# Performance work log

Hardware: AMD Instinct MI355X
Metric: run time of the kernel (lower is better)

Reference implementation:

```python
import jax, jax.numpy as jnp
import numpy as np

B, S, N, F_IN = 4, 256, 500, 32
D, L = 64, 2
TEMP = 0.5
EPS = 1e-5

def gelu(x):
    return jax.nn.gelu(x, approximate=False)  # torch default GELU (erf)

def layernorm(h, g, b):
    mu = h.mean(-1, keepdims=True)
    var = ((h - mu) ** 2).mean(-1, keepdims=True)
    return (h - mu) * jax.lax.rsqrt(var + EPS) * g + b

def gru_last(x_seq, Wih, Whh, bih, bhh):
    # x_seq: [B, T, I]; torch nn.GRU gate math, h0 = 0; returns final hidden [B, D]
    xp = jnp.einsum('bti,gi->btg', x_seq, Wih) + bih  # precompute input gates [B, T, 3D]
    d = Whh.shape[1]
    def step(h, xpt):
        gh = h @ Whh.T + bhh
        xr, xz, xn = jnp.split(xpt, 3, axis=-1)
        hr, hz, hn = jnp.split(gh, 3, axis=-1)
        r = jax.nn.sigmoid(xr + hr)
        z = jax.nn.sigmoid(xz + hz)
        n = jnp.tanh(xn + r * hn)
        return (1.0 - z) * n + z * h, None
    h0 = jnp.zeros((x_seq.shape[0], d), x_seq.dtype)
    h, _ = jax.lax.scan(step, h0, xp.transpose(1, 0, 2))
    return h

def forward(x, ip_W, ip_b, from_embed, to_embed, gl_W, gl_b, gl_g, gl_be,
            Wih_s, Whh_s, bih_s, bhh_s, Wih_m, Whh_m, bih_m, bhh_m,
            Wih_l, Whh_l, bih_l, bhh_l, dh_W1, dh_b1, dh_W2, dh_b2):
    # input_proj: Linear + GELU (Dropout is identity in eval)
    x = gelu(jnp.einsum('bsnf,df->bsnd', x, ip_W) + ip_b)  # [B,S,N,D]
    # learned adjacency: softmax over destination nodes
    adj = jax.nn.softmax((from_embed @ to_embed.T) / TEMP, axis=-1)  # [N,N]
    for i in range(gl_W.shape[0]):
        agg = jnp.einsum('bsnd,nm->bsmd', x, adj)
        h = gelu(jnp.einsum('bsnd,ed->bsne', x + agg, gl_W[i]) + gl_b[i])
        x = layernorm(h, gl_g[i], gl_be[i])
    b, s, n, d = x.shape
    x_flat = x.reshape(b, s, n * d)
    h_s = gru_last(x_flat[:, -10:, :], Wih_s, Whh_s, bih_s, bhh_s)
    h_m = gru_last(x_flat[:, -20:, :], Wih_m, Whh_m, bih_m, bhh_m)
    h_l = gru_last(x_flat, Wih_l, Whh_l, bih_l, bhh_l)
    h = jnp.concatenate([h_s, h_m, h_l], axis=-1)  # [B, 3D]
    h = gelu(h @ dh_W1.T + dh_b1)
    return h @ dh_W2.T + dh_b2  # direction logits [B, N]

def setup_inputs():
    key = jax.random.key(0)
    it = iter(jax.random.split(key, 40))
    rn = lambda shape, s=0.02: jax.random.normal(next(it), shape, jnp.float32) * s
    I = N * D
    return {
        'x': jax.random.normal(next(it), (B, S, N, F_IN), jnp.float32),
        'ip_W': rn((D, F_IN)), 'ip_b': jnp.zeros((D,), jnp.float32),
        'from_embed': rn((N, 32), 0.1), 'to_embed': rn((N, 32), 0.1),
        'gl_W': rn((L, D, D)), 'gl_b': jnp.zeros((L, D), jnp.float32),
        'gl_g': jnp.ones((L, D), jnp.float32), 'gl_be': jnp.zeros((L, D), jnp.float32),
        'Wih_s': rn((3 * D, I)), 'Whh_s': rn((3 * D, D)),
        'bih_s': jnp.zeros((3 * D,), jnp.float32), 'bhh_s': jnp.zeros((3 * D,), jnp.float32),
        'Wih_m': rn((3 * D, I)), 'Whh_m': rn((3 * D, D)),
        'bih_m': jnp.zeros((3 * D,), jnp.float32), 'bhh_m': jnp.zeros((3 * D,), jnp.float32),
        'Wih_l': rn((3 * D, I)), 'Whh_l': rn((3 * D, D)),
        'bih_l': jnp.zeros((3 * D,), jnp.float32), 'bhh_l': jnp.zeros((3 * D,), jnp.float32),
        'dh_W1': rn((D, 3 * D)), 'dh_b1': jnp.zeros((D,), jnp.float32),
        'dh_W2': rn((N, D)), 'dh_b2': jnp.zeros((N,), jnp.float32),
    }

def reference(x, ip_W, ip_b, from_embed, to_embed, gl_W, gl_b, gl_g, gl_be,
              Wih_s, Whh_s, bih_s, bhh_s, Wih_m, Whh_m, bih_m, bhh_m,
              Wih_l, Whh_l, bih_l, bhh_l, dh_W1, dh_b1, dh_W2, dh_b2):
    return forward(x, ip_W, ip_b, from_embed, to_embed, gl_W, gl_b, gl_g, gl_be,
                   Wih_s, Whh_s, bih_s, bhh_s, Wih_m, Whh_m, bih_m, bhh_m,
                   Wih_l, Whh_l, bih_l, bhh_l, dh_W1, dh_b1, dh_W2, dh_b2)
```

## Files before the change

### kernel.cpp

```cpp
#include <hip/hip_runtime.h>
#include <math.h>

#define NN 500
#define DD 64
#define NPAD 512
#define COLS 65536
#define BS_TOT 1024
#define I_DIM 32000
#define KS_GRU 40
#define KSL 800

typedef __attribute__((ext_vector_type(8))) short bf16x8;
typedef __attribute__((ext_vector_type(4))) float f32x4;

__device__ __forceinline__ float gelu_f(float x) {
    return 0.5f * x * (1.0f + erff(x * 0.70710678118654752440f));
}

__device__ __forceinline__ unsigned short bf16_rn(float x) {
    unsigned int u = __float_as_uint(x);
    unsigned int r = u + 0x7FFFu + ((u >> 16) & 1u);
    return (unsigned short)(r >> 16);
}
__device__ __forceinline__ float bf16_tof(unsigned short h) {
    return __uint_as_float(((unsigned int)h) << 16);
}
__device__ __forceinline__ unsigned int pack_hl(float x) {
    unsigned short h = bf16_rn(x);
    unsigned short l = bf16_rn(x - bf16_tof(h));
    return (unsigned int)h | ((unsigned int)l << 16);
}
__device__ __forceinline__ float unpack_val(unsigned int u) {
    return __uint_as_float(u << 16) + __uint_as_float(u & 0xFFFF0000u);
}
__device__ __forceinline__ void split4(float4 v, short4& h4, short4& l4) {
    h4.x = (short)bf16_rn(v.x); l4.x = (short)bf16_rn(v.x - bf16_tof((unsigned short)h4.x));
    h4.y = (short)bf16_rn(v.y); l4.y = (short)bf16_rn(v.y - bf16_tof((unsigned short)h4.y));
    h4.z = (short)bf16_rn(v.z); l4.z = (short)bf16_rn(v.z - bf16_tof((unsigned short)h4.z));
    h4.w = (short)bf16_rn(v.w); l4.w = (short)bf16_rn(v.w - bf16_tof((unsigned short)h4.w));
}

__device__ __forceinline__ int swz_k(int row, int kbyte) {
    return kbyte ^ (((row >> 3) & 3) << 4);
}

__global__ __launch_bounds__(512)
void adj_kernel(const float* __restrict__ fe, const float* __restrict__ te,
                short* __restrict__ adjTh, short* __restrict__ adjTl)
{
    __shared__ float fr[32];
    __shared__ float red[8];
    __shared__ float red2[8];
    const int n = blockIdx.x;
    const int tid = threadIdx.x;
    if (tid < 32) fr[tid] = fe[n * 32 + tid];
    __syncthreads();
    const int m = tid;
    float s = -1e30f;
    if (m < NN) {
        float acc = 0.f;
        #pragma unroll
        for (int f = 0; f < 32; ++f) acc += fr[f] * te[m * 32 + f];
        s = acc * 2.0f;
    }
    float v = s;
    #pragma unroll
    for (int off = 32; off; off >>= 1) v = fmaxf(v, __shfl_xor(v, off));
    if ((tid & 63) == 0) red[tid >> 6] = v;
    __syncthreads();
    float bmax = red[0];
    #pragma unroll
    for (int i = 1; i < 8; ++i) bmax = fmaxf(bmax, red[i]);
    float e = (m < NN) ? expf(s - bmax) : 0.f;
    float v2 = e;
    #pragma unroll
    for (int off = 32; off; off >>= 1) v2 += __shfl_xor(v2, off);
    if ((tid & 63) == 0) red2[tid >> 6] = v2;
    __syncthreads();
    float bsum = 0.f;
    #pragma unroll
    for (int i = 0; i < 8; ++i) bsum += red2[i];
    if (m < NN) {
        float p = e / bsum;
        unsigned short h = bf16_rn(p);
        adjTh[(size_t)m * NPAD + n] = (short)h;
        adjTl[(size_t)m * NPAD + n] = (short)bf16_rn(p - bf16_tof(h));
    }
}

__global__ __launch_bounds__(256)
void wsplit_kernel(const float* __restrict__ W, short* __restrict__ H,
                   short* __restrict__ L, int n4)
{
    int i = blockIdx.x * 256 + threadIdx.x;
    if (i < n4) {
        float4 v = *(const float4*)&W[i * 4];
        short4 h4, l4;
        split4(v, h4, l4);
        *(short4*)&H[i * 4] = h4;
        *(short4*)&L[i * 4] = l4;
    }
}

__global__ __launch_bounds__(256)
void proj_mfma_kernel(const float* __restrict__ xin,
                      const short* __restrict__ Wh, const short* __restrict__ Wl,
                      const float* __restrict__ ipb, unsigned int* __restrict__ Xhl)
{
    const int tid  = threadIdx.x;
    const int lane = tid & 63;
    const int wave = tid >> 6;
    const int q = lane >> 4, r16 = lane & 15;
    const size_t row0 = (size_t)blockIdx.x * 128 + wave * 32;

    float bB[4];
    #pragma unroll
    for (int ci = 0; ci < 4; ++ci) bB[ci] = ipb[ci * 16 + r16];

    bf16x8 wh[4], wl[4];
    #pragma unroll
    for (int ci = 0; ci < 4; ++ci) {
        int off = (ci * 16 + r16) * 32 + q * 8;
        wh[ci] = *(const bf16x8*)&Wh[off];
        wl[ci] = *(const bf16x8*)&Wl[off];
    }

    f32x4 acc[2][4];
    #pragma unroll
    for (int i = 0; i < 2; ++i)
        #pragma unroll
        for (int j = 0; j < 4; ++j) acc[i][j] = (f32x4){0.f, 0.f, 0.f, 0.f};

    #pragma unroll
    for (int mi = 0; mi < 2; ++mi) {
        const size_t row = row0 + mi * 16 + r16;
        const int n = (int)(row >> 10), bs = (int)(row & 1023);
        const float* src = &xin[((size_t)bs * NN + n) * 32 + q * 8];
        float4 v0 = *(const float4*)src;
        float4 v1 = *(const float4*)(src + 4);
        short4 h0, l0, h1, l1;
        split4(v0, h0, l0);
        split4(v1, h1, l1);
        bf16x8 ah, al;
        ah[0] = h0.x; ah[1] = h0.y; ah[2] = h0.z; ah[3] = h0.w;
        ah[4] = h1.x; ah[5] = h1.y; ah[6] = h1.z; ah[7] = h1.w;
        al[0] = l0.x; al[1] = l0.y; al[2] = l0.z; al[3] = l0.w;
        al[4] = l1.x; al[5] = l1.y; al[6] = l1.z; al[7] = l1.w;
        #pragma unroll
        for (int ci = 0; ci < 4; ++ci) {
            acc[mi][ci] = __builtin_amdgcn_mfma_f32_16x16x32_bf16(ah, wh[ci], acc[mi][ci], 0, 0, 0);
            acc[mi][ci] = __builtin_amdgcn_mfma_f32_16x16x32_bf16(ah, wl[ci], acc[mi][ci], 0, 0, 0);
            acc[mi][ci] = __builtin_amdgcn_mfma_f32_16x16x32_bf16(al, wh[ci], acc[mi][ci], 0, 0, 0);
        }
    }

    #pragma unroll
    for (int mi = 0; mi < 2; ++mi) {
        #pragma unroll
        for (int rg = 0; rg < 4; ++rg) {
            size_t grow = row0 + mi * 16 + q * 4 + rg;
            #pragma unroll
            for (int ci = 0; ci < 4; ++ci) {
                float y = gelu_f(acc[mi][ci][rg] + bB[ci]);
                Xhl[grow * 64 + ci * 16 + r16] = pack_hl(y);
            }
        }
    }
}

__global__ __launch_bounds__(256)
void agg_mfma_kernel(const unsigned int* __restrict__ Xhl,
                     const short* __restrict__ adjTh, const short* __restrict__ adjTl,
                     unsigned int* __restrict__ Yhl)
{
    __shared__ __align__(16) short Ah[2][128 * 40];
    __shared__ __align__(16) short Al[2][128 * 40];
    __shared__ __align__(16) short Bh[2][128 * 40];
    __shared__ __align__(16) short Bl[2][128 * 40];

    const int tid  = threadIdx.x;
    const int lane = tid & 63;
    const int wave = tid >> 6;
    const int wm = (wave >> 1) * 64;
    const int wc = (wave & 1) * 64;
    const int q = lane >> 4, r16 = lane & 15;
    const int c0 = blockIdx.x * 128;
    const int m0 = blockIdx.y * 128;

    const int sa_m = tid >> 1, sa_kh = tid & 1;
    const int sb_c = tid & 127, sb_kh = tid >> 7;
    const size_t cb = (size_t)(c0 + sb_c);

    f32x4 acc[4][4];
    #pragma unroll
    for (int i = 0; i < 4; ++i)
        #pragma unroll
        for (int j = 0; j < 4; ++j) acc[i][j] = (f32x4){0.f, 0.f, 0.f, 0.f};

    {
        const size_t base = (size_t)(m0 + sa_m) * NPAD + sa_kh * 16;
        bf16x8 h0 = *(const bf16x8*)&adjTh[base];
        bf16x8 h1 = *(const bf16x8*)&adjTh[base + 8];
        bf16x8 l0 = *(const bf16x8*)&adjTl[base];
        bf16x8 l1 = *(const bf16x8*)&adjTl[base + 8];
        char* rowH = (char*)Ah[0] + sa_m * 80;
        char* rowL = (char*)Al[0] + sa_m * 80;
        *(bf16x8*)(rowH + swz_k(sa_m, sa_kh * 32))      = h0;
        *(bf16x8*)(rowH + swz_k(sa_m, sa_kh * 32 + 16)) = h1;
        *(bf16x8*)(rowL + swz_k(sa_m, sa_kh * 32))      = l0;
        *(bf16x8*)(rowL + swz_k(sa_m, sa_kh * 32 + 16)) = l1;

        unsigned int u[16];
        #pragma unroll
        for (int j = 0; j < 16; ++j) {
            int kk = sb_kh * 16 + j;
            u[j] = (kk < NN) ? Xhl[(size_t)kk * COLS + cb] : 0u;
        }
        bf16x8 bh0, bh1, bl0, bl1;
        #pragma unroll
        for (int j = 0; j < 8; ++j) {
            bh0[j] = (short)(u[j] & 0xFFFFu);     bl0[j] = (short)(u[j] >> 16);
            bh1[j] = (short)(u[8 + j] & 0xFFFFu); bl1[j] = (short)(u[8 + j] >> 16);
        }
        char* rbH = (char*)Bh[0] + sb_c * 80;
        char* rbL = (char*)Bl[0] + sb_c * 80;
        int kb0 = swz_k(sb_c, sb_kh * 32);
        int kb1 = swz_k(sb_c, sb_kh * 32 + 16);
        *(bf16x8*)(rbH + kb0) = bh0; *(bf16x8*)(rbH + kb1) = bh1;
        *(bf16x8*)(rbL + kb0) = bl0; *(bf16x8*)(rbL + kb1) = bl1;
    }
    __syncthreads();

    for (int kc = 0; kc < 16; ++kc) {
        const int cur = kc & 1;
        bf16x8 nAh0, nAh1, nAl0, nAl1;
        unsigned int nu[16];
        if (kc < 15) {
            const int k0n = (kc + 1) * 32;
            const size_t base = (size_t)(m0 + sa_m) * NPAD + k0n + sa_kh * 16;
            nAh0 = *(const bf16x8*)&adjTh[base];
            nAh1 = *(const bf16x8*)&adjTh[base + 8];
            nAl0 = *(const bf16x8*)&adjTl[base];
            nAl1 = *(const bf16x8*)&adjTl[base + 8];
            #pragma unroll
            for (int j = 0; j < 16; ++j) {
                int kk = k0n + sb_kh * 16 + j;
                nu[j] = (kk < NN) ? Xhl[(size_t)kk * COLS + cb] : 0u;
            }
        }
        bf16x8 ah[4], al[4];
        #pragma unroll
        for (int mi = 0; mi < 4; ++mi) {
            int row = wm + mi * 16 + r16;
            int kb = swz_k(row, q * 16);
            ah[mi] = *(const bf16x8*)((const char*)Ah[cur] + row * 80 + kb);
            al[mi] = *(const bf16x8*)((const char*)Al[cur] + row * 80 + kb);
        }
        #pragma unroll
        for (int ci = 0; ci < 4; ++ci) {
            int row = wc + ci * 16 + r16;
            int kb = swz_k(row, q * 16);
            bf16x8 bh = *(const bf16x8*)((const char*)Bh[cur] + row * 80 + kb);
            bf16x8 bl = *(const bf16x8*)((const char*)Bl[cur] + row * 80 + kb);
            #pragma unroll
            for (int mi = 0; mi < 4; ++mi) {
                acc[mi][ci] = __builtin_amdgcn_mfma_f32_16x16x32_bf16(ah[mi], bh, acc[mi][ci], 0, 0, 0);
                acc[mi][ci] = __builtin_amdgcn_mfma_f32_16x16x32_bf16(ah[mi], bl, acc[mi][ci], 0, 0, 0);
                acc[mi][ci] = __builtin_amdgcn_mfma_f32_16x16x32_bf16(al[mi], bh, acc[mi][ci], 0, 0, 0);
            }
        }
        if (kc < 15) {
            const int nb = cur ^ 1;
            char* rowH = (char*)Ah[nb] + sa_m * 80;
            char* rowL = (char*)Al[nb] + sa_m * 80;
            *(bf16x8*)(rowH + swz_k(sa_m, sa_kh * 32))      = nAh0;
            *(bf16x8*)(rowH + swz_k(sa_m, sa_kh * 32 + 16)) = nAh1;
            *(bf16x8*)(rowL + swz_k(sa_m, sa_kh * 32))      = nAl0;
            *(bf16x8*)(rowL + swz_k(sa_m, sa_kh * 32 + 16)) = nAl1;
            bf16x8 bh0, bh1, bl0, bl1;
            #pragma unroll
            for (int j = 0; j < 8; ++j) {
                bh0[j] = (short)(nu[j] & 0xFFFFu);     bl0[j] = (short)(nu[j] >> 16);
                bh1[j] = (short)(nu[8 + j] & 0xFFFFu); bl1[j] = (short)(nu[8 + j] >> 16);
            }
            char* rbH = (char*)Bh[nb] + sb_c * 80;
            char* rbL = (char*)Bl[nb] + sb_c * 80;
            int kb0 = swz_k(sb_c, sb_kh * 32);
            int kb1 = swz_k(sb_c, sb_kh * 32 + 16);
            *(bf16x8*)(rbH + kb0) = bh0; *(bf16x8*)(rbH + kb1) = bh1;
            *(bf16x8*)(rbL + kb0) = bl0; *(bf16x8*)(rbL + kb1) = bl1;
        }
        __syncthreads();
    }

    #pragma unroll
    for (int mi = 0; mi < 4; ++mi) {
        #pragma unroll
        for (int r = 0; r < 4; ++r) {
            int m = m0 + wm + mi * 16 + q * 4 + r;
            if (m < NN) {
                #pragma unroll
                for (int ci = 0; ci < 4; ++ci) {
                    size_t idx = (size_t)m * COLS + c0 + wc + ci * 16 + r16;
                    float y = acc[mi][ci][r] + unpack_val(Xhl[idx]);
                    Yhl[idx] = pack_hl(y);
                }
            }
        }
    }
}

__global__ __launch_bounds__(256)
void hln_stream_kernel(unsigned int* __restrict__ Xio,
                       const short* __restrict__ Wh, const short* __restrict__ Wl,
                       const float* __restrict__ glb, const float* __restrict__ glg,
                       const float* __restrict__ glbe)
{
    const int tid  = threadIdx.x;
    const int lane = tid & 63;
    const int wave = tid >> 6;
    const int q = lane >> 4, r16 = lane & 15;
    const size_t row0 = (size_t)blockIdx.x * 128 + wave * 32;

    float bB2[4], bG2[4], bE2[4];
    #pragma unroll
    for (int ci = 0; ci < 4; ++ci) {
        int e = ci * 16 + r16;
        bB2[ci] = glb[e]; bG2[ci] = glg[e]; bE2[ci] = glbe[e];
    }

    f32x4 acc[2][4];
    #pragma unroll
    for (int i = 0; i < 2; ++i)
        #pragma unroll
        for (int j = 0; j < 4; ++j) acc[i][j] = (f32x4){0.f, 0.f, 0.f, 0.f};

    #pragma unroll
    for (int kh = 0; kh < 2; ++kh) {
        bf16x8 wh[4], wl[4];
        #pragma unroll
        for (int ci = 0; ci < 4; ++ci) {
            int off = (ci * 16 + r16) * 64 + kh * 32 + q * 8;
            wh[ci] = *(const bf16x8*)&Wh[off];
            wl[ci] = *(const bf16x8*)&Wl[off];
        }
        #pragma unroll
        for (int mi = 0; mi < 2; ++mi) {
            const size_t row = row0 + mi * 16 + r16;
            const unsigned int* src = &Xio[row * 64 + kh * 32 + q * 8];
            uint4 u0 = *(const uint4*)src;
            uint4 u1 = *(const uint4*)(src + 4);
            bf16x8 ah, al;
            ah[0] = (short)(u0.x & 0xFFFFu); al[0] = (short)(u0.x >> 16);
            ah[1] = (short)(u0.y & 0xFFFFu); al[1] = (short)(u0.y >> 16);
            ah[2] = (short)(u0.z & 0xFFFFu); al[2] = (short)(u0.z >> 16);
            ah[3] = (short)(u0.w & 0xFFFFu); al[3] = (short)(u0.w >> 16);
            ah[4] = (short)(u1.x & 0xFFFFu); al[4] = (short)(u1.x >> 16);
            ah[5] = (short)(u1.y & 0xFFFFu); al[5] = (short)(u1.y >> 16);
            ah[6] = (short)(u1.z & 0xFFFFu); al[6] = (short)(u1.z >> 16);
            ah[7] = (short)(u1.w & 0xFFFFu); al[7] = (short)(u1.w >> 16);
            #pragma unroll
            for (int ci = 0; ci < 4; ++ci) {
                acc[mi][ci] = __builtin_amdgcn_mfma_f32_16x16x32_bf16(ah, wh[ci], acc[mi][ci], 0, 0, 0);
                acc[mi][ci] = __builtin_amdgcn_mfma_f32_16x16x32_bf16(ah, wl[ci], acc[mi][ci], 0, 0, 0);
                acc[mi][ci] = __builtin_amdgcn_mfma_f32_16x16x32_bf16(al, wh[ci], acc[mi][ci], 0, 0, 0);
            }
        }
    }

    #pragma unroll
    for (int mi = 0; mi < 2; ++mi) {
        #pragma unroll
        for (int rg = 0; rg < 4; ++rg) {
            float h[4];
            float s1 = 0.f;
            #pragma unroll
            for (int ci = 0; ci < 4; ++ci) {
                h[ci] = gelu_f(acc[mi][ci][rg] + bB2[ci]);
                s1 += h[ci];
            }
            #pragma unroll
            for (int off = 1; off < 16; off <<= 1) s1 += __shfl_xor(s1, off);
            float mu = s1 * (1.f / 64.f);
            float s2 = 0.f;
            #pragma unroll
            for (int ci = 0; ci < 4; ++ci) { float dc = h[ci] - mu; s2 += dc * dc; }
            #pragma unroll
            for (int off = 1; off < 16; off <<= 1) s2 += __shfl_xor(s2, off);
            float rs = 1.f / sqrtf(s2 * (1.f / 64.f) + 1e-5f);
            size_t grow = row0 + mi * 16 + q * 4 + rg;
            #pragma unroll
            for (int ci = 0; ci < 4; ++ci) {
                float y = (h[ci] - mu) * rs * bG2[ci] + bE2[ci];
                Xio[grow * 64 + ci * 16 + r16] = pack_hl(y);
            }
        }
    }
}

__global__ __launch_bounds__(256)
void wconv_kernel(const float* __restrict__ W0, const float* __restrict__ W1,
                  const float* __restrict__ W2,
                  short* __restrict__ h0, short* __restrict__ l0,
                  short* __restrict__ h1, short* __restrict__ l1,
                  short* __restrict__ h2, short* __restrict__ l2)
{
    const int gi = blockIdx.y;
    const float* W = (gi == 0) ? W0 : (gi == 1) ? W1 : W2;
    short* H = (gi == 0) ? h0 : (gi == 1) ? h1 : h2;
    short* L = (gi == 0) ? l0 : (gi == 1) ? l1 : l2;
    const size_t i = ((size_t)blockIdx.x * 256 + threadIdx.x) * 4;
    float4 v = *(const float4*)&W[i];
    short4 h4, l4;
    split4(v, h4, l4);
    *(short4*)&H[i] = h4;
    *(short4*)&L[i] = l4;
}

__global__ __launch_bounds__(256)
void gru_pre_mfma_kernel(const unsigned int* __restrict__ Xhl,
                         const short* __restrict__ Wh0, const short* __restrict__ Wl0,
                         const short* __restrict__ Wh1, const short* __restrict__ Wl1,
                         const short* __restrict__ Wh2, const short* __restrict__ Wl2,
                         float* __restrict__ p0, float* __restrict__ p1,
                         float* __restrict__ p2)
{
    __shared__ __align__(16) short Ah[64 * 40];
    __shared__ __align__(16) short Al[64 * 40];
    __shared__ __align__(16) short Bh[192 * 40];
    __shared__ __align__(16) short Bl[192 * 40];

    const int bid = blockIdx.x;
    int gi, mtid, ks;
    if (bid < 40)       { gi = 0; mtid = 0;             ks = bid; }
    else if (bid < 120) { int r = bid - 40;  gi = 1; ks = r % 40; mtid = r / 40; }
    else                { int r = bid - 120; gi = 2; ks = r % 40; mtid = r / 40; }
    const short* Wh = (gi == 0) ? Wh0 : (gi == 1) ? Wh1 : Wh2;
    const short* Wl = (gi == 0) ? Wl0 : (gi == 1) ? Wl1 : Wl2;
    float* partial  = (gi == 0) ? p0 : (gi == 1) ? p1 : p2;
    const int Trows = (gi == 0) ? 10 : (gi == 1) ? 20 : 256;
    const int toff  = (gi == 0) ? 246 : (gi == 1) ? 236 : 0;
    const int M     = (gi == 0) ? 40 : (gi == 1) ? 80 : 1024;
    const int R0 = mtid * 64;

    const int tid  = threadIdx.x;
    const int lane = tid & 63;
    const int wave = tid >> 6;
    const int wr = (wave & 1) * 32;
    const int wg = (wave >> 1) * 96;
    const int q = lane >> 4, r16 = lane & 15;

    const int sa_r = tid >> 2, sa_kq = tid & 3;
    const bool vldA = (R0 + sa_r < M);
    int btA = 0;
    if (vldA) { int R = R0 + sa_r; int b = R / Trows, t = R - b * Trows; btA = b * 256 + toff + t; }

    f32x4 acc[2][6];
    #pragma unroll
    for (int i = 0; i < 2; ++i)
        #pragma unroll
        for (int j = 0; j < 6; ++j) acc[i][j] = (f32x4){0.f, 0.f, 0.f, 0.f};

    for (int c = 0; c < KSL / 32; ++c) {
        const int k0 = ks * KSL + c * 32;
        {
            const int kk = k0 + sa_kq * 8;
            const int nn = kk >> 6, d0 = kk & 63;
            uint4 u0 = make_uint4(0u, 0u, 0u, 0u), u1 = u0;
            if (vldA) {
                const unsigned int* src = &Xhl[((size_t)nn * BS_TOT + btA) * 64 + d0];
                u0 = *(const uint4*)src;
                u1 = *(const uint4*)(src + 4);
            }
            short4 h0 = make_short4((short)(u0.x & 0xFFFF), (short)(u0.y & 0xFFFF),
                                    (short)(u0.z & 0xFFFF), (short)(u0.w & 0xFFFF));
            short4 l0 = make_short4((short)(u0.x >> 16), (short)(u0.y >> 16),
                                    (short)(u0.z >> 16), (short)(u0.w >> 16));
            short4 h1 = make_short4((short)(u1.x & 0xFFFF), (short)(u1.y & 0xFFFF),
                                    (short)(u1.z & 0xFFFF), (short)(u1.w & 0xFFFF));
            short4 l1 = make_short4((short)(u1.x >> 16), (short)(u1.y >> 16),
                                    (short)(u1.z >> 16), (short)(u1.w >> 16));
            int kb = swz_k(sa_r, sa_kq * 16);
            char* rowH = (char*)Ah + sa_r * 80;
            char* rowL = (char*)Al + sa_r * 80;
            *(short4*)(rowH + kb) = h0; *(short4*)(rowH + kb + 8) = h1;
            *(short4*)(rowL + kb) = l0; *(short4*)(rowL + kb + 8) = l1;
        }
        #pragma unroll
        for (int l = 0; l < 3; ++l) {
            int idx = tid + l * 256;
            int g = idx >> 2, kq = idx & 3;
            const size_t src = (size_t)g * I_DIM + k0 + kq * 8;
            bf16x8 hv = *(const bf16x8*)&Wh[src];
            bf16x8 lv = *(const bf16x8*)&Wl[src];
            int kb = swz_k(g, kq * 16);
            *(bf16x8*)((char*)Bh + g * 80 + kb) = hv;
            *(bf16x8*)((char*)Bl + g * 80 + kb) = lv;
        }
        __syncthreads();
        bf16x8 ah[2], al[2];
        #pragma unroll
        for (int mi = 0; mi < 2; ++mi) {
            int row = wr + mi * 16 + r16;
            int kb = swz_k(row, q * 16);
            ah[mi] = *(const bf16x8*)((const char*)Ah + row * 80 + kb);
            al[mi] = *(const bf16x8*)((const char*)Al + row * 80 + kb);
        }
        #pragma unroll
        for (int ci = 0; ci < 6; ++ci) {
            int grow = wg + ci * 16 + r16;
            int kb = swz_k(grow, q * 16);
            bf16x8 bh = *(const bf16x8*)((const char*)Bh + grow * 80 + kb);
            bf16x8 bl = *(const bf16x8*)((const char*)Bl + grow * 80 + kb);
            #pragma unroll
            for (int mi = 0; mi < 2; ++mi) {
                acc[mi][ci] = __builtin_amdgcn_mfma_f32_16x16x32_bf16(ah[mi], bh, acc[mi][ci], 0, 0, 0);
                acc[mi][ci] = __builtin_amdgcn_mfma_f32_16x16x32_bf16(ah[mi], bl, acc[mi][ci], 0, 0, 0);
                acc[mi][ci] = __builtin_amdgcn_mfma_f32_16x16x32_bf16(al[mi], bh, acc[mi][ci], 0, 0, 0);
            }
        }
        __syncthreads();
    }
    #pragma unroll
    for (int mi = 0; mi < 2; ++mi) {
        #pragma unroll
        for (int r = 0; r < 4; ++r) {
            int R = R0 + wr + mi * 16 + q * 4 + r;
            if (R < M) {
                #pragma unroll
                for (int ci = 0; ci < 6; ++ci)
                    partial[((size_t)ks * M + R) * 192 + wg + ci * 16 + r16] = acc[mi][ci][r];
            }
        }
    }
}

__global__ __launch_bounds__(192)
void gru_reduce_fused_kernel(const float* __restrict__ p0, const float* __restrict__ p1,
                             const float* __restrict__ p2,
                             const float* __restrict__ bih0, const float* __restrict__ bih1,
                             const float* __restrict__ bih2,
                             float* __restrict__ xp0, float* __restrict__ xp1,
                             float* __restrict__ xp2)
{
    int r = blockIdx.x;
    const float* partial; const float* bih; float* xp; int M;
    if (r < 40)       { partial = p0; bih = bih0; xp = xp0; M = 40; }
    else if (r < 120) { r -= 40;  partial = p1; bih = bih1; xp = xp1; M = 80; }
    else              { r -= 120; partial = p2; bih = bih2; xp = xp2; M = 1024; }
    const int g = threadIdx.x;
    float acc = bih[g];
    for (int ks = 0; ks < KS_GRU; ++ks)
        acc += partial[((size_t)ks * M + r) * 192 + g];
    xp[(size_t)r * 192 + g] = acc;
}

__global__ __launch_bounds__(192)
void gru_scan_kernel(const float* __restrict__ xp_s, const float* __restrict__ xp_m,
                     const float* __restrict__ xp_l,
                     const float* __restrict__ Whh_s, const float* __restrict__ Whh_m,
                     const float* __restrict__ Whh_l,
                     const float* __restrict__ bhh_s, const float* __restrict__ bhh_m,
                     const float* __restrict__ bhh_l,
                     float* __restrict__ hcat)
{
    __shared__ float h[64];
    __shared__ float gh[192];
    const int blk = blockIdx.x;
    const int g3 = blk >> 2, b = blk & 3;
    const float* xp  = (g3 == 0) ? xp_s : (g3 == 1) ? xp_m : xp_l;
    const float* Whh = (g3 == 0) ? Whh_s : (g3 == 1) ? Whh_m : Whh_l;
    const float* bhh = (g3 == 0) ? bhh_s : (g3 == 1) ? bhh_m : bhh_l;
    const int T = (g3 == 0) ? 10 : (g3 == 1) ? 20 : 256;
    const int g = threadIdx.x;

    float w[64];
    #pragma unroll
    for (int k4 = 0; k4 < 16; ++k4) {
        float4 v = *(const float4*)&Whh[g * 64 + k4 * 4];
        w[k4 * 4 + 0] = v.x; w[k4 * 4 + 1] = v.y;
        w[k4 * 4 + 2] = v.z; w[k4 * 4 + 3] = v.w;
    }
    const float bh = bhh[g];
    if (g < 64) h[g] = 0.f;

    const float* xpb = xp + (size_t)b * T * 192;
    float xr_c = 0.f, xz_c = 0.f, xn_c = 0.f;
    if (g < 64) { xr_c = xpb[g]; xz_c = xpb[64 + g]; xn_c = xpb[128 + g]; }
    __syncthreads();

    for (int t = 0; t < T; ++t) {
        float xr_n = 0.f, xz_n = 0.f, xn_n = 0.f;
        if (t + 1 < T && g < 64) {
            const float* xq = xpb + (size_t)(t + 1) * 192;
            xr_n = xq[g]; xz_n = xq[64 + g]; xn_n = xq[128 + g];
        }
        float a0 = 0.f, a1 = 0.f, a2 = 0.f, a3 = 0.f;
        #pragma unroll
        for (int k4 = 0; k4 < 16; ++k4) {
            float4 hv = ((const float4*)h)[k4];
            a0 += hv.x * w[k4 * 4 + 0];
            a1 += hv.y * w[k4 * 4 + 1];
            a2 += hv.z * w[k4 * 4 + 2];
            a3 += hv.w * w[k4 * 4 + 3];
        }
        gh[g] = bh + ((a0 + a1) + (a2 + a3));
        __syncthreads();
        if (g < 64) {
            float hr = gh[g], hz = gh[64 + g], hn = gh[128 + g];
            float r = 1.f / (1.f + __expf(-(xr_c + hr)));
            float z = 1.f / (1.f + __expf(-(xz_c + hz)));
            float pre = xn_c + r * hn;
            float e2 = __expf(2.f * pre);
            float nv = 1.f - 2.f / (e2 + 1.f);
            h[g] = (1.f - z) * nv + z * h[g];
        }
        __syncthreads();
        xr_c = xr_n; xz_c = xz_n; xn_c = xn_n;
    }
    if (g < 64) hcat[b * 192 + g3 * 64 + g] = h[g];
}

__global__ __launch_bounds__(512)
void head_kernel(const float* __restrict__ hcat,
                 const float* __restrict__ W1, const float* __restrict__ b1,
                 const float* __restrict__ W2, const float* __restrict__ b2,
                 float* __restrict__ out)
{
    __shared__ float hc[4][192];
    __shared__ float h1[4][64];
    const int tid = threadIdx.x;
    for (int i = tid; i < 768; i += 512) hc[i / 192][i % 192] = hcat[i];
    __syncthreads();
    if (tid < 256) {
        int b = tid >> 6, e = tid & 63;
        float acc = b1[e];
        #pragma unroll
        for (int k = 0; k < 192; ++k) acc += hc[b][k] * W1[e * 192 + k];
        h1[b][e] = gelu_f(acc);
    }
    __syncthreads();
    for (int o = tid; o < 2000; o += 512) {
        int b = o / 500, n = o % 500;
        float acc = b2[n];
        #pragma unroll
        for (int k = 0; k < 64; ++k) acc += h1[b][k] * W2[n * 64 + k];
        out[o] = acc;
    }
}

extern "C" void kernel_launch(void* const* d_in, const int* in_sizes, int n_in,
                              void* d_out, int out_size, void* d_ws, size_t ws_size,
                              hipStream_t stream)
{
    (void)in_sizes; (void)n_in; (void)out_size; (void)ws_size;
    const float* x    = (const float*)d_in[0];
    const float* ipW  = (const float*)d_in[1];
    const float* ipb  = (const float*)d_in[2];
    const float* fe   = (const float*)d_in[3];
    const float* te   = (const float*)d_in[4];
    const float* glW  = (const float*)d_in[5];
    const float* glb  = (const float*)d_in[6];
    const float* glg  = (const float*)d_in[7];
    const float* glbe = (const float*)d_in[8];
    const float* Wih[3] = {(const float*)d_in[9],  (const float*)d_in[13], (const float*)d_in[17]};
    const float* Whh[3] = {(const float*)d_in[10], (const float*)d_in[14], (const float*)d_in[18]};
    const float* bih[3] = {(const float*)d_in[11], (const float*)d_in[15], (const float*)d_in[19]};
    const float* bhh[3] = {(const float*)d_in[12], (const float*)d_in[16], (const float*)d_in[20]};
    const float* W1 = (const float*)d_in[21];
    const float* b1 = (const float*)d_in[22];
    const float* W2 = (const float*)d_in[23];
    const float* b2 = (const float*)d_in[24];
    float* out = (float*)d_out;

    unsigned int* Xhl = (unsigned int*)d_ws;
    unsigned int* Yhl = Xhl + 32768000;
    short* adjTh = (short*)(Yhl + 32768000);
    short* adjTl = adjTh + NPAD * NPAD;
    short* glWh  = adjTl + NPAD * NPAD;
    short* glWl  = glWh + 8192;
    short* ipWh  = glWl + 8192;
    short* ipWl  = ipWh + 2048;
    short* wbase = (short*)Yhl;
    short* Wh0 = wbase;
    short* Wl0 = Wh0 + 6144000;
    short* Wh1 = Wl0 + 6144000;
    short* Wl1 = Wh1 + 6144000;
    short* Wh2 = Wl1 + 6144000;
    short* Wl2 = Wh2 + 6144000;
    float* pbase = (float*)Yhl + 18432000;
    float* part0 = pbase;
    float* part1 = part0 + 307200;
    float* part2 = part1 + 614400;
    float* xp0   = part2 + 7864320;
    float* xp1   = xp0 + 7680;
    float* xp2   = xp1 + 15360;
    float* hcat  = xp2 + 196608;

    hipMemsetAsync(adjTh, 0, (size_t)NPAD * NPAD * 2 * sizeof(short), stream);
    adj_kernel<<<NN, 512, 0, stream>>>(fe, te, adjTh, adjTl);
    wsplit_kernel<<<8, 256, 0, stream>>>(glW, glWh, glWl, 2048);
    wsplit_kernel<<<2, 256, 0, stream>>>(ipW, ipWh, ipWl, 512);
    proj_mfma_kernel<<<4000, 256, 0, stream>>>(x, ipWh, ipWl, ipb, Xhl);

    agg_mfma_kernel<<<dim3(512, 4), 256, 0, stream>>>(Xhl, adjTh, adjTl, Yhl);
    hln_stream_kernel<<<4000, 256, 0, stream>>>(Yhl, glWh, glWl, glb, glg, glbe);
    agg_mfma_kernel<<<dim3(512, 4), 256, 0, stream>>>(Yhl, adjTh, adjTl, Xhl);
    hln_stream_kernel<<<4000, 256, 0, stream>>>(Xhl, glWh + 4096, glWl + 4096,
                                                glb + 64, glg + 64, glbe + 64);

    wconv_kernel<<<dim3(6000, 3), 256, 0, stream>>>(Wih[0], Wih[1], Wih[2],
                                                    Wh0, Wl0, Wh1, Wl1, Wh2, Wl2);
    gru_pre_mfma_kernel<<<760, 256, 0, stream>>>(Xhl, Wh0, Wl0, Wh1, Wl1, Wh2, Wl2,
                                                 part0, part1, part2);
    gru_reduce_fused_kernel<<<1144, 192, 0, stream>>>(part0, part1, part2,
                                                      bih[0], bih[1], bih[2],
                                                      xp0, xp1, xp2);
    gru_scan_kernel<<<12, 192, 0, stream>>>(xp0, xp1, xp2,
                                            Whh[0], Whh[1], Whh[2],
                                            bhh[0], bhh[1], bhh[2], hcat);
    head_kernel<<<1, 512, 0, stream>>>(hcat, W1, b1, W2, b2, out);
}
```

Baseline: 768.7 us.

## Load adjacency fragments directly from global and swap agg grid order

The aggregation kernel no longer stages the adjacency (A) tiles through double-buffered shared memory. Each wave now loads its MFMA A fragments straight from global memory, relying on the cache because the adjacency matrix is small and reused by every block. The grid is also transposed so that the four row-tile blocks sharing a column tile run next to each other, which improves L2 reuse of the X column data. This cuts LDS traffic and usage, which may raise occupancy, but the A loads are no longer prefetched a step ahead, so global latency sits directly on the MFMA path.

```diff
diff --git a/kernel.cpp b/kernel.cpp
--- a/kernel.cpp
+++ b/kernel.cpp
@@ -173,8 +173,6 @@
                      const short* __restrict__ adjTh, const short* __restrict__ adjTl,
                      unsigned int* __restrict__ Yhl)
 {
-    __shared__ __align__(16) short Ah[2][128 * 40];
-    __shared__ __align__(16) short Al[2][128 * 40];
     __shared__ __align__(16) short Bh[2][128 * 40];
     __shared__ __align__(16) short Bl[2][128 * 40];
 
@@ -184,10 +182,9 @@
     const int wm = (wave >> 1) * 64;
     const int wc = (wave & 1) * 64;
     const int q = lane >> 4, r16 = lane & 15;
-    const int c0 = blockIdx.x * 128;
-    const int m0 = blockIdx.y * 128;
-
-    const int sa_m = tid >> 1, sa_kh = tid & 1;
+    const int m0 = blockIdx.x * 128;
+    const int c0 = blockIdx.y * 128;
+
     const int sb_c = tid & 127, sb_kh = tid >> 7;
     const size_t cb = (size_t)(c0 + sb_c);
 
@@ -198,18 +195,6 @@
         for (int j = 0; j < 4; ++j) acc[i][j] = (f32x4){0.f, 0.f, 0.f, 0.f};
 
     {
-        const size_t base = (size_t)(m0 + sa_m) * NPAD + sa_kh * 16;
-        bf16x8 h0 = *(const bf16x8*)&adjTh[base];
-        bf16x8 h1 = *(const bf16x8*)&adjTh[base + 8];
-        bf16x8 l0 = *(const bf16x8*)&adjTl[base];
-        bf16x8 l1 = *(const bf16x8*)&adjTl[base + 8];
-        char* rowH = (char*)Ah[0] + sa_m * 80;
-        char* rowL = (char*)Al[0] + sa_m * 80;
-        *(bf16x8*)(rowH + swz_k(sa_m, sa_kh * 32))      = h0;
-        *(bf16x8*)(rowH + swz_k(sa_m, sa_kh * 32 + 16)) = h1;
-        *(bf16x8*)(rowL + swz_k(sa_m, sa_kh * 32))      = l0;
-        *(bf16x8*)(rowL + swz_k(sa_m, sa_kh * 32 + 16)) = l1;
-
         unsigned int u[16];
         #pragma unroll
         for (int j = 0; j < 16; ++j) {
@@ -233,15 +218,10 @@
 
     for (int kc = 0; kc < 16; ++kc) {
         const int cur = kc & 1;
-        bf16x8 nAh0, nAh1, nAl0, nAl1;
+        const int k0 = kc * 32;
         unsigned int nu[16];
         if (kc < 15) {
-            const int k0n = (kc + 1) * 32;
-            const size_t base = (size_t)(m0 + sa_m) * NPAD + k0n + sa_kh * 16;
-            nAh0 = *(const bf16x8*)&adjTh[base];
-            nAh1 = *(const bf16x8*)&adjTh[base + 8];
-            nAl0 = *(const bf16x8*)&adjTl[base];
-            nAl1 = *(const bf16x8*)&adjTl[base + 8];
+            const int k0n = k0 + 32;
             #pragma unroll
             for (int j = 0; j < 16; ++j) {
                 int kk = k0n + sb_kh * 16 + j;
@@ -251,10 +231,9 @@
         bf16x8 ah[4], al[4];
         #pragma unroll
         for (int mi = 0; mi < 4; ++mi) {
-            int row = wm + mi * 16 + r16;
-            int kb = swz_k(row, q * 16);
-            ah[mi] = *(const bf16x8*)((const char*)Ah[cur] + row * 80 + kb);
-            al[mi] = *(const bf16x8*)((const char*)Al[cur] + row * 80 + kb);
+            const size_t base = (size_t)(m0 + wm + mi * 16 + r16) * NPAD + k0 + q * 8;
+            ah[mi] = *(const bf16x8*)&adjTh[base];
+            al[mi] = *(const bf16x8*)&adjTl[base];
         }
         #pragma unroll
         for (int ci = 0; ci < 4; ++ci) {
@@ -271,12 +250,6 @@
         }
         if (kc < 15) {
             const int nb = cur ^ 1;
-            char* rowH = (char*)Ah[nb] + sa_m * 80;
-            char* rowL = (char*)Al[nb] + sa_m * 80;
-            *(bf16x8*)(rowH + swz_k(sa_m, sa_kh * 32))      = nAh0;
-            *(bf16x8*)(rowH + swz_k(sa_m, sa_kh * 32 + 16)) = nAh1;
-            *(bf16x8*)(rowL + swz_k(sa_m, sa_kh * 32))      = nAl0;
-            *(bf16x8*)(rowL + swz_k(sa_m, sa_kh * 32 + 16)) = nAl1;
             bf16x8 bh0, bh1, bl0, bl1;
             #pragma unroll
             for (int j = 0; j < 8; ++j) {
@@ -703,9 +676,9 @@
     wsplit_kernel<<<2, 256, 0, stream>>>(ipW, ipWh, ipWl, 512);
     proj_mfma_kernel<<<4000, 256, 0, stream>>>(x, ipWh, ipWl, ipb, Xhl);
 
-    agg_mfma_kernel<<<dim3(512, 4), 256, 0, stream>>>(Xhl, adjTh, adjTl, Yhl);
+    agg_mfma_kernel<<<dim3(4, 512), 256, 0, stream>>>(Xhl, adjTh, adjTl, Yhl);
     hln_stream_kernel<<<4000, 256, 0, stream>>>(Yhl, glWh, glWl, glb, glg, glbe);
-    agg_mfma_kernel<<<dim3(512, 4), 256, 0, stream>>>(Yhl, adjTh, adjTl, Xhl);
+    agg_mfma_kernel<<<dim3(4, 512), 256, 0, stream>>>(Yhl, adjTh, adjTl, Xhl);
     hln_stream_kernel<<<4000, 256, 0, stream>>>(Xhl, glWh + 4096, glWl + 4096,
                                                 glb + 64, glg + 64, glbe + 64);
 
```

New measurement: 890.2 us. 15.8% more time.
